# Optimization experiments

Hardware: AMD Instinct MI355X
Metric: run time of the kernel (lower is better)

Reference implementation:

```python
import jax, jax.numpy as jnp
import numpy as np


def _block(x, W, b, use_relu):
    # x: (B, n, dx). Faithful to PairwiseInteractions: full pairwise L2 dist,
    # top-k (k == n) smallest sorted, drop self, concat(self, neighbor), linear,
    # optional relu, mean over the n-1 neighbors.
    B, n, dx = x.shape
    sq = jnp.sum(x * x, axis=-1)                                   # (B, n)
    d2 = sq[:, :, None] + sq[:, None, :] - 2.0 * jnp.einsum('bnd,bmd->bnm', x, x)
    dist = jnp.sqrt(jnp.maximum(d2, 0.0))                          # (B, n, n)
    _, idx = jax.lax.top_k(-dist, n)                               # ascending distances
    idx_nb = idx[:, :, 1:]                                         # drop self -> (B, n, n-1)
    nbr = jnp.take_along_axis(x[:, None, :, :], idx_nb[..., None], axis=2)  # (B, n, n-1, dx)
    self_rep = jnp.broadcast_to(x[:, :, None, :], nbr.shape)
    pairs = jnp.concatenate([self_rep, nbr], axis=-1)              # (B, n, n-1, 2*dx)
    h = pairs @ W + b
    if use_relu:
        h = jax.nn.relu(h)
    return jnp.sum(h, axis=2) / (n - 1)                            # (B, n, d_out)


def setup_inputs() -> dict:
    key = jax.random.key(0)
    ks = jax.random.split(key, 4)
    B, N, d = 2, 1024, 3

    def lin(k, fin, fout):
        kw, kb = jax.random.split(k)
        lim = 1.0 / np.sqrt(fin).astype(np.float32)
        W = jax.random.uniform(kw, (fin, fout), minval=-lim, maxval=lim, dtype=jnp.float32)
        b = jax.random.uniform(kb, (fout,), minval=-lim, maxval=lim, dtype=jnp.float32)
        return W, b

    W1, b1 = lin(ks[1], 2 * d, 32)
    W2, b2 = lin(ks[2], 2 * 32, 64)
    W3, b3 = lin(ks[3], 2 * 64, d)
    x = jax.random.normal(ks[0], (B, N * d), dtype=jnp.float32)
    return {"x": x, "W1": W1, "b1": b1, "W2": W2, "b2": b2, "W3": W3, "b3": b3}


def reference(x, W1, b1, W2, b2, W3, b3):
    B = x.shape[0]
    d = W3.shape[1]
    N = x.shape[1] // d
    h = x.reshape(B, N, d)
    h = _block(h, W1, b1, True)    # eb1: d -> 32, relu
    h = _block(h, W2, b2, True)    # eb2: 32 -> 64, relu
    h = _block(h, W3, b3, False)   # eb3: 64 -> d, no relu
    return h.reshape(B, N * d)
```

## Files before the change

### kernel.cpp

```cpp
#include <hip/hip_runtime.h>

#define BB 2
#define NN 1024

__global__ void k_ac1(const float* __restrict__ x, const float* __restrict__ W1,
                      const float* __restrict__ b1,
                      float* __restrict__ a1, float* __restrict__ c1) {
    int t = blockIdx.x * blockDim.x + threadIdx.x;
    int i = t >> 5, f = t & 31;
    float x0 = x[i * 3 + 0], x1 = x[i * 3 + 1], x2 = x[i * 3 + 2];
    float a = x0 * W1[0 * 32 + f] + x1 * W1[1 * 32 + f] + x2 * W1[2 * 32 + f];
    float c = x0 * W1[3 * 32 + f] + x1 * W1[4 * 32 + f] + x2 * W1[5 * 32 + f] + b1[f];
    a1[t] = a;
    c1[t] = c;
}

__global__ __launch_bounds__(256) void k_pair32(const float* __restrict__ a1,
                                                const float* __restrict__ c1,
                                                float* __restrict__ out1) {
    __shared__ float cbuf[256 * 32];
    int wave = threadIdx.x >> 6;
    int lane = threadIdx.x & 63;
    int js = lane >> 5, f = lane & 31;
    int i = blockIdx.x * 4 + wave;
    int b = i >> 10;
    const float* cb = c1 + b * (NN * 32);
    float a = a1[i * 32 + f];
    float acc = 0.f;
    for (int tile = 0; tile < NN; tile += 256) {
        const float4* src = (const float4*)(cb + tile * 32);
        float4* dst = (float4*)cbuf;
        for (int k = threadIdx.x; k < 2048; k += 256) dst[k] = src[k];
        __syncthreads();
        #pragma unroll 8
        for (int jj = js; jj < 256; jj += 2) {
            acc += fmaxf(a + cbuf[jj * 32 + f], 0.f);
        }
        __syncthreads();
    }
    acc += __shfl_xor(acc, 32);
    float self = fmaxf(a + c1[i * 32 + f], 0.f);
    float res = (acc - self) / 1023.0f;
    if (js == 0) out1[i * 32 + f] = res;
}

__global__ void k_ac2(const float* __restrict__ h, const float* __restrict__ W2,
                      const float* __restrict__ b2,
                      float* __restrict__ a2, float* __restrict__ c2) {
    int t = blockIdx.x * blockDim.x + threadIdx.x;
    int i = t >> 6, f = t & 63;
    const float* hr = h + i * 32;
    float a = 0.f, c = b2[f];
    #pragma unroll
    for (int d = 0; d < 32; ++d) {
        float hv = hr[d];
        a += hv * W2[d * 64 + f];
        c += hv * W2[(32 + d) * 64 + f];
    }
    a2[t] = a;
    c2[t] = c;
}

__global__ __launch_bounds__(256) void k_pair64(const float* __restrict__ a2,
                                                const float* __restrict__ c2,
                                                float* __restrict__ out2) {
    __shared__ float cbuf[128 * 64];
    int wave = threadIdx.x >> 6;
    int lane = threadIdx.x & 63;
    int i = blockIdx.x * 4 + wave;
    int b = i >> 10;
    const float* cb = c2 + b * (NN * 64);
    float a = a2[i * 64 + lane];
    float acc = 0.f;
    for (int tile = 0; tile < NN; tile += 128) {
        const float4* src = (const float4*)(cb + tile * 64);
        float4* dst = (float4*)cbuf;
        for (int k = threadIdx.x; k < 2048; k += 256) dst[k] = src[k];
        __syncthreads();
        #pragma unroll 8
        for (int jj = 0; jj < 128; ++jj) {
            acc += fmaxf(a + cbuf[jj * 64 + lane], 0.f);
        }
        __syncthreads();
    }
    float self = fmaxf(a + c2[i * 64 + lane], 0.f);
    out2[i * 64 + lane] = (acc - self) / 1023.0f;
}

__global__ void k_colsum(const float* __restrict__ out2, const float* __restrict__ W3,
                         float* __restrict__ S) {
    __shared__ float part[4][64];
    __shared__ float colsum[64];
    int b = blockIdx.x;
    int t = threadIdx.x;
    int d = t & 63, chunk = t >> 6;
    const float* base = out2 + b * (NN * 64);
    float s = 0.f;
    for (int j = chunk * 256; j < chunk * 256 + 256; ++j) s += base[j * 64 + d];
    part[chunk][d] = s;
    __syncthreads();
    if (t < 64) colsum[t] = part[0][t] + part[1][t] + part[2][t] + part[3][t];
    __syncthreads();
    if (t < 3) {
        float acc = 0.f;
        for (int d2 = 0; d2 < 64; ++d2) acc += colsum[d2] * W3[(64 + d2) * 3 + t];
        S[b * 3 + t] = acc;
    }
}

__global__ void k_final(const float* __restrict__ out2, const float* __restrict__ W3,
                        const float* __restrict__ b3, const float* __restrict__ S,
                        float* __restrict__ out) {
    int t = blockIdx.x * blockDim.x + threadIdx.x;
    int b = t >> 10;
    const float* row = out2 + t * 64;
    float a0 = 0, a1 = 0, a2 = 0, c0 = 0, c1 = 0, c2 = 0;
    #pragma unroll
    for (int d = 0; d < 64; ++d) {
        float v = row[d];
        a0 += v * W3[d * 3 + 0];
        a1 += v * W3[d * 3 + 1];
        a2 += v * W3[d * 3 + 2];
        c0 += v * W3[(64 + d) * 3 + 0];
        c1 += v * W3[(64 + d) * 3 + 1];
        c2 += v * W3[(64 + d) * 3 + 2];
    }
    float* o = out + t * 3;
    o[0] = a0 + b3[0] + (S[b * 3 + 0] - c0) / 1023.0f;
    o[1] = a1 + b3[1] + (S[b * 3 + 1] - c1) / 1023.0f;
    o[2] = a2 + b3[2] + (S[b * 3 + 2] - c2) / 1023.0f;
}

extern "C" void kernel_launch(void* const* d_in, const int* in_sizes, int n_in,
                              void* d_out, int out_size, void* d_ws, size_t ws_size,
                              hipStream_t stream) {
    const float* x  = (const float*)d_in[0];
    const float* W1 = (const float*)d_in[1];
    const float* b1 = (const float*)d_in[2];
    const float* W2 = (const float*)d_in[3];
    const float* b2 = (const float*)d_in[4];
    const float* W3 = (const float*)d_in[5];
    const float* b3 = (const float*)d_in[6];
    float* out = (float*)d_out;

    float* ws = (float*)d_ws;
    float* a1   = ws;
    float* c1   = a1 + 2048 * 32;
    float* out1 = c1 + 2048 * 32;
    float* a2   = out1 + 2048 * 32;
    float* c2   = a2 + 2048 * 64;
    float* out2 = c2 + 2048 * 64;
    float* S    = out2 + 2048 * 64;

    k_ac1<<<(2048 * 32) / 256, 256, 0, stream>>>(x, W1, b1, a1, c1);
    k_pair32<<<512, 256, 0, stream>>>(a1, c1, out1);
    k_ac2<<<(2048 * 64) / 256, 256, 0, stream>>>(out1, W2, b2, a2, c2);
    k_pair64<<<512, 256, 0, stream>>>(a2, c2, out2);
    k_colsum<<<2, 256, 0, stream>>>(out2, W3, S);
    k_final<<<2048 / 256, 256, 0, stream>>>(out2, W3, b3, S, out);
}
```

Before: 122.0 us.

## Fuse all stages into one cooperative kernel with grid syncs

```diff
diff --git a/kernel.cpp b/kernel.cpp
--- a/kernel.cpp
+++ b/kernel.cpp
@@ -1,134 +1,132 @@
 #include <hip/hip_runtime.h>
+#include <hip/hip_cooperative_groups.h>
 
-#define BB 2
+namespace cg = cooperative_groups;
+
 #define NN 1024
 
-__global__ void k_ac1(const float* __restrict__ x, const float* __restrict__ W1,
-                      const float* __restrict__ b1,
-                      float* __restrict__ a1, float* __restrict__ c1) {
-    int t = blockIdx.x * blockDim.x + threadIdx.x;
-    int i = t >> 5, f = t & 31;
-    float x0 = x[i * 3 + 0], x1 = x[i * 3 + 1], x2 = x[i * 3 + 2];
-    float a = x0 * W1[0 * 32 + f] + x1 * W1[1 * 32 + f] + x2 * W1[2 * 32 + f];
-    float c = x0 * W1[3 * 32 + f] + x1 * W1[4 * 32 + f] + x2 * W1[5 * 32 + f] + b1[f];
-    a1[t] = a;
-    c1[t] = c;
-}
+__global__ __launch_bounds__(256) void fused_net(
+    const float* __restrict__ x,  const float* __restrict__ W1, const float* __restrict__ b1,
+    const float* __restrict__ W2, const float* __restrict__ b2,
+    const float* __restrict__ W3, const float* __restrict__ b3,
+    float* __restrict__ out,
+    float* __restrict__ out1, float* __restrict__ a2g, float* __restrict__ c2g,
+    float* __restrict__ out2, float* __restrict__ partials)
+{
+    cg::grid_group grid = cg::this_grid();
+    __shared__ float cbuf[8192];
+    __shared__ float pcol[4][64];
+    __shared__ float sS[4];
 
-__global__ __launch_bounds__(256) void k_pair32(const float* __restrict__ a1,
-                                                const float* __restrict__ c1,
-                                                float* __restrict__ out1) {
-    __shared__ float cbuf[256 * 32];
-    int wave = threadIdx.x >> 6;
-    int lane = threadIdx.x & 63;
-    int js = lane >> 5, f = lane & 31;
-    int i = blockIdx.x * 4 + wave;
-    int b = i >> 10;
-    const float* cb = c1 + b * (NN * 32);
-    float a = a1[i * 32 + f];
-    float acc = 0.f;
-    for (int tile = 0; tile < NN; tile += 256) {
-        const float4* src = (const float4*)(cb + tile * 32);
-        float4* dst = (float4*)cbuf;
-        for (int k = threadIdx.x; k < 2048; k += 256) dst[k] = src[k];
+    const int tid  = threadIdx.x;
+    const int wave = tid >> 6, lane = tid & 63;
+    const int blk  = blockIdx.x;
+
+    {
+        int i  = blk * 4 + wave;
+        int b  = i >> 10;
+        int il = i & 1023;
+        int js = lane >> 5, f = lane & 31;
+        const float* xb = x + b * (NN * 3);
+        float xi0 = xb[il*3+0], xi1 = xb[il*3+1], xi2 = xb[il*3+2];
+        float a     = xi0*W1[0*32+f] + xi1*W1[1*32+f] + xi2*W1[2*32+f];
+        float cself = xi0*W1[3*32+f] + xi1*W1[4*32+f] + xi2*W1[5*32+f] + b1[f];
+        float acc = 0.f;
+        int f2 = tid & 31, r0 = tid >> 5;
+        float w3f = W1[3*32+f2], w4f = W1[4*32+f2], w5f = W1[5*32+f2], bf = b1[f2];
+        for (int tile = 0; tile < NN; tile += 256) {
+            #pragma unroll 4
+            for (int k = 0; k < 32; ++k) {
+                int r = tile + r0 + k*8;
+                float y0 = xb[r*3+0], y1 = xb[r*3+1], y2 = xb[r*3+2];
+                cbuf[(r0 + k*8)*32 + f2] = y0*w3f + y1*w4f + y2*w5f + bf;
+            }
+            __syncthreads();
+            #pragma unroll 8
+            for (int jj = js; jj < 256; jj += 2)
+                acc += fmaxf(a + cbuf[jj*32 + f], 0.f);
+            __syncthreads();
+        }
+        acc += __shfl_xor(acc, 32);
+        float res = (acc - fmaxf(a + cself, 0.f)) * (1.0f/1023.0f);
+        if (js == 0) out1[i*32 + f] = res;
+    }
+    grid.sync();
+
+    {
+        int t = blk * 256 + tid;
+        int i = t >> 6, f = t & 63;
+        const float* hr = out1 + i * 32;
+        float a = 0.f, c = b2[f];
+        #pragma unroll
+        for (int d = 0; d < 32; ++d) {
+            float hv = hr[d];
+            a += hv * W2[d*64 + f];
+            c += hv * W2[(32 + d)*64 + f];
+        }
+        a2g[t] = a;
+        c2g[t] = c;
+    }
+    grid.sync();
+
+    {
+        int i = blk * 4 + wave;
+        int b = i >> 10;
+        const float* cb = c2g + b * (NN * 64);
+        float a = a2g[i*64 + lane];
+        float acc = 0.f;
+        for (int tile = 0; tile < NN; tile += 128) {
+            const float4* src = (const float4*)(cb + tile * 64);
+            float4* dst = (float4*)cbuf;
+            for (int k = tid; k < 2048; k += 256) dst[k] = src[k];
+            __syncthreads();
+            #pragma unroll 8
+            for (int jj = 0; jj < 128; ++jj)
+                acc += fmaxf(a + cbuf[jj*64 + lane], 0.f);
+            __syncthreads();
+        }
+        float res = (acc - fmaxf(a + c2g[i*64 + lane], 0.f)) * (1.0f/1023.0f);
+        out2[i*64 + lane] = res;
+        pcol[wave][lane] = res;
         __syncthreads();
-        #pragma unroll 8
-        for (int jj = js; jj < 256; jj += 2) {
-            acc += fmaxf(a + cbuf[jj * 32 + f], 0.f);
+        if (tid < 64)
+            partials[blk*64 + tid] = pcol[0][tid] + pcol[1][tid] + pcol[2][tid] + pcol[3][tid];
+    }
+    grid.sync();
+
+    if (blk < 8) {
+        int b = blk >> 2;
+        {
+            int col = tid & 63, q = tid >> 6;
+            float s = 0.f;
+            const float* pb = partials + b * 256 * 64;
+            #pragma unroll 8
+            for (int k = q*64; k < q*64 + 64; ++k) s += pb[k*64 + col];
+            pcol[q][col] = s;
         }
         __syncthreads();
-    }
-    acc += __shfl_xor(acc, 32);
-    float self = fmaxf(a + c1[i * 32 + f], 0.f);
-    float res = (acc - self) / 1023.0f;
-    if (js == 0) out1[i * 32 + f] = res;
-}
-
-__global__ void k_ac2(const float* __restrict__ h, const float* __restrict__ W2,
-                      const float* __restrict__ b2,
-                      float* __restrict__ a2, float* __restrict__ c2) {
-    int t = blockIdx.x * blockDim.x + threadIdx.x;
-    int i = t >> 6, f = t & 63;
-    const float* hr = h + i * 32;
-    float a = 0.f, c = b2[f];
-    #pragma unroll
-    for (int d = 0; d < 32; ++d) {
-        float hv = hr[d];
-        a += hv * W2[d * 64 + f];
-        c += hv * W2[(32 + d) * 64 + f];
-    }
-    a2[t] = a;
-    c2[t] = c;
-}
-
-__global__ __launch_bounds__(256) void k_pair64(const float* __restrict__ a2,
-                                                const float* __restrict__ c2,
-                                                float* __restrict__ out2) {
-    __shared__ float cbuf[128 * 64];
-    int wave = threadIdx.x >> 6;
-    int lane = threadIdx.x & 63;
-    int i = blockIdx.x * 4 + wave;
-    int b = i >> 10;
-    const float* cb = c2 + b * (NN * 64);
-    float a = a2[i * 64 + lane];
-    float acc = 0.f;
-    for (int tile = 0; tile < NN; tile += 128) {
-        const float4* src = (const float4*)(cb + tile * 64);
-        float4* dst = (float4*)cbuf;
-        for (int k = threadIdx.x; k < 2048; k += 256) dst[k] = src[k];
-        __syncthreads();
-        #pragma unroll 8
-        for (int jj = 0; jj < 128; ++jj) {
-            acc += fmaxf(a + cbuf[jj * 64 + lane], 0.f);
+        if (wave < 3) {
+            float cs = pcol[0][lane] + pcol[1][lane] + pcol[2][lane] + pcol[3][lane];
+            float p = cs * W3[(64 + lane)*3 + wave];
+            #pragma unroll
+            for (int off = 32; off; off >>= 1) p += __shfl_xor(p, off);
+            if (lane == 0) sS[wave] = p;
         }
         __syncthreads();
+        int t = blk * 256 + tid;
+        const float* row = out2 + t * 64;
+        float r0 = 0, r1 = 0, r2 = 0, q0 = 0, q1 = 0, q2 = 0;
+        #pragma unroll
+        for (int d = 0; d < 64; ++d) {
+            float v = row[d];
+            r0 += v * W3[d*3+0];       r1 += v * W3[d*3+1];       r2 += v * W3[d*3+2];
+            q0 += v * W3[(64+d)*3+0];  q1 += v * W3[(64+d)*3+1];  q2 += v * W3[(64+d)*3+2];
+        }
+        float* o = out + t * 3;
+        o[0] = r0 + b3[0] + (sS[0] - q0) * (1.0f/1023.0f);
+        o[1] = r1 + b3[1] + (sS[1] - q1) * (1.0f/1023.0f);
+        o[2] = r2 + b3[2] + (sS[2] - q2) * (1.0f/1023.0f);
     }
-    float self = fmaxf(a + c2[i * 64 + lane], 0.f);
-    out2[i * 64 + lane] = (acc - self) / 1023.0f;
-}
-
-__global__ void k_colsum(const float* __restrict__ out2, const float* __restrict__ W3,
-                         float* __restrict__ S) {
-    __shared__ float part[4][64];
-    __shared__ float colsum[64];
-    int b = blockIdx.x;
-    int t = threadIdx.x;
-    int d = t & 63, chunk = t >> 6;
-    const float* base = out2 + b * (NN * 64);
-    float s = 0.f;
-    for (int j = chunk * 256; j < chunk * 256 + 256; ++j) s += base[j * 64 + d];
-    part[chunk][d] = s;
-    __syncthreads();
-    if (t < 64) colsum[t] = part[0][t] + part[1][t] + part[2][t] + part[3][t];
-    __syncthreads();
-    if (t < 3) {
-        float acc = 0.f;
-        for (int d2 = 0; d2 < 64; ++d2) acc += colsum[d2] * W3[(64 + d2) * 3 + t];
-        S[b * 3 + t] = acc;
-    }
-}
-
-__global__ void k_final(const float* __restrict__ out2, const float* __restrict__ W3,
-                        const float* __restrict__ b3, const float* __restrict__ S,
-                        float* __restrict__ out) {
-    int t = blockIdx.x * blockDim.x + threadIdx.x;
-    int b = t >> 10;
-    const float* row = out2 + t * 64;
-    float a0 = 0, a1 = 0, a2 = 0, c0 = 0, c1 = 0, c2 = 0;
-    #pragma unroll
-    for (int d = 0; d < 64; ++d) {
-        float v = row[d];
-        a0 += v * W3[d * 3 + 0];
-        a1 += v * W3[d * 3 + 1];
-        a2 += v * W3[d * 3 + 2];
-        c0 += v * W3[(64 + d) * 3 + 0];
-        c1 += v * W3[(64 + d) * 3 + 1];
-        c2 += v * W3[(64 + d) * 3 + 2];
-    }
-    float* o = out + t * 3;
-    o[0] = a0 + b3[0] + (S[b * 3 + 0] - c0) / 1023.0f;
-    o[1] = a1 + b3[1] + (S[b * 3 + 1] - c1) / 1023.0f;
-    o[2] = a2 + b3[2] + (S[b * 3 + 2] - c2) / 1023.0f;
 }
 
 extern "C" void kernel_launch(void* const* d_in, const int* in_sizes, int n_in,
@@ -144,18 +142,14 @@
     float* out = (float*)d_out;
 
     float* ws = (float*)d_ws;
-    float* a1   = ws;
-    float* c1   = a1 + 2048 * 32;
-    float* out1 = c1 + 2048 * 32;
-    float* a2   = out1 + 2048 * 32;
-    float* c2   = a2 + 2048 * 64;
-    float* out2 = c2 + 2048 * 64;
-    float* S    = out2 + 2048 * 64;
+    float* out1     = ws;
+    float* a2g      = out1 + 2048*32;
+    float* c2g      = a2g  + 2048*64;
+    float* out2     = c2g  + 2048*64;
+    float* partials = out2 + 2048*64;
 
-    k_ac1<<<(2048 * 32) / 256, 256, 0, stream>>>(x, W1, b1, a1, c1);
-    k_pair32<<<512, 256, 0, stream>>>(a1, c1, out1);
-    k_ac2<<<(2048 * 64) / 256, 256, 0, stream>>>(out1, W2, b2, a2, c2);
-    k_pair64<<<512, 256, 0, stream>>>(a2, c2, out2);
-    k_colsum<<<2, 256, 0, stream>>>(out2, W3, S);
-    k_final<<<2048 / 256, 256, 0, stream>>>(out2, W3, b3, S, out);
+    void* args[] = { (void*)&x, (void*)&W1, (void*)&b1, (void*)&W2, (void*)&b2,
+                     (void*)&W3, (void*)&b3, (void*)&out,
+                     (void*)&out1, (void*)&a2g, (void*)&c2g, (void*)&out2, (void*)&partials };
+    hipLaunchCooperativeKernel((void*)fused_net, dim3(512), dim3(256), args, 0, stream);
 }
```

After: 272.7 us. 2.24x slower.
